# Performance work log

Hardware: AMD Instinct MI355X
Metric: run time of the kernel (lower is better)

Reference implementation:

```python
import jax, jax.numpy as jnp
import numpy as np

D_IN = 1024
D_OUT = 1024


def setup_inputs() -> dict:
    key = jax.random.key(0)
    ks = jax.random.split(key, 7)
    x = jax.random.normal(ks[0], (4, 2048, D_IN), dtype=jnp.float32)
    scale = 1.0 / np.sqrt(D_IN)
    Wq = jax.random.normal(ks[1], (D_IN, D_OUT), dtype=jnp.float32) * scale
    Wk = jax.random.normal(ks[2], (D_IN, D_OUT), dtype=jnp.float32) * scale
    Wv = jax.random.normal(ks[3], (D_IN, D_OUT), dtype=jnp.float32) * scale
    bq = jax.random.normal(ks[4], (D_OUT,), dtype=jnp.float32) * 0.01
    bk = jax.random.normal(ks[5], (D_OUT,), dtype=jnp.float32) * 0.01
    bv = jax.random.normal(ks[6], (D_OUT,), dtype=jnp.float32) * 0.01
    return {"x": x, "Wq": Wq, "bq": bq, "Wk": Wk, "bk": bk, "Wv": Wv, "bv": bv}


def reference(x, Wq, bq, Wk, bk, Wv, bv):
    # x: [B, S, d_in]
    q = jnp.einsum("bsd,de->bse", x, Wq) + bq  # [B, S, d_out]
    k = jnp.einsum("bsd,de->bse", x, Wk) + bk
    v = jnp.einsum("bsd,de->bse", x, Wv) + bv
    d_out = q.shape[-1]
    scores = jnp.einsum("bqe,bke->bqk", q, k) / jnp.sqrt(jnp.float32(d_out))
    attn = jax.nn.softmax(scores, axis=-1)  # [B, S, S]
    return jnp.einsum("bqk,bke->bqe", attn, v)
```

## Files before the change

kernel.cpp:

```cpp
#include <hip/hip_runtime.h>
#include <hip/hip_bf16.h>
#include <stdint.h>

typedef __bf16 bf16x8 __attribute__((ext_vector_type(8)));
typedef __bf16 bf16x4 __attribute__((ext_vector_type(4)));
typedef float f32x4 __attribute__((ext_vector_type(4)));

#define DEV __device__ __forceinline__

DEV void gload_lds16(const void* g, void* l) {
  __builtin_amdgcn_global_load_lds((const __attribute__((address_space(1))) void*)g,
                                   (__attribute__((address_space(3))) void*)l, 16, 0, 0);
}

#define WAITV0 asm volatile("s_waitcnt vmcnt(0)" ::: "memory")
#define MFMA16x16(a, b, c) __builtin_amdgcn_mfma_f32_16x16x32_bf16(a, b, c, 0, 0, 0)

__global__ __launch_bounds__(256) void pack_x_kernel(const float* __restrict__ x,
                                                     __bf16* __restrict__ o, long n) {
  long i = ((long)blockIdx.x * 256 + threadIdx.x) * 4;
  const long stride = (long)gridDim.x * 256 * 4;
  for (; i < n; i += stride) {
    f32x4 v = *(const f32x4*)(x + i);
    bf16x4 b;
    b[0] = (__bf16)v[0]; b[1] = (__bf16)v[1]; b[2] = (__bf16)v[2]; b[3] = (__bf16)v[3];
    *(bf16x4*)(o + i) = b;
  }
}

__global__ __launch_bounds__(256) void pack_w_kernel(const float* __restrict__ Wq,
                                                     const float* __restrict__ Wk,
                                                     const float* __restrict__ Wv,
                                                     __bf16* __restrict__ Wt) {
  const int w = blockIdx.z;
  const float* W = (w == 0) ? Wq : (w == 1) ? Wk : Wv;
  const float scale = (w == 0) ? 0.03125f : 1.0f;
  const int d0 = blockIdx.x * 64;
  const int e0 = blockIdx.y * 64;
  __shared__ __bf16 T[64][72];
  const int tid = threadIdx.x;
  const int r4 = tid >> 4;
  const int c4 = (tid & 15) * 4;
#pragma unroll
  for (int p = 0; p < 4; ++p) {
    int r = r4 + p * 16;
    f32x4 v = *(const f32x4*)(W + (long)(d0 + r) * 1024 + e0 + c4);
    T[r][c4 + 0] = (__bf16)(v[0] * scale);
    T[r][c4 + 1] = (__bf16)(v[1] * scale);
    T[r][c4 + 2] = (__bf16)(v[2] * scale);
    T[r][c4 + 3] = (__bf16)(v[3] * scale);
  }
  __syncthreads();
  const int e4 = tid >> 3;
  const int dd = (tid & 7) * 8;
#pragma unroll
  for (int p = 0; p < 2; ++p) {
    int e = e4 + p * 32;
    bf16x8 ov;
#pragma unroll
    for (int j = 0; j < 8; ++j) ov[j] = T[dd + j][e];
    *(bf16x8*)(Wt + (long)w * 1048576 + (long)(e0 + e) * 1024 + d0 + dd) = ov;
  }
}

__global__ __launch_bounds__(256) void pack_bias_kernel(const float* __restrict__ bq,
                                                        const float* __restrict__ bk,
                                                        const float* __restrict__ bv,
                                                        float* __restrict__ o) {
  int i = blockIdx.x * 256 + threadIdx.x;
  if (i < 1024) o[i] = bq[i] * 0.03125f;
  else if (i < 2048) o[i] = bk[i - 1024];
  else if (i < 3072) o[i] = bv[i - 2048];
}

template <int MODE>
__global__ __launch_bounds__(256, 2) void gemm_bk32_kernel(
    const __bf16* __restrict__ A, int lda,
    const __bf16* __restrict__ B, int ldb, long long bBatchStride, int bmShift,
    const float* __restrict__ bias,
    __bf16* __restrict__ C, int ldc,
    __bf16* __restrict__ vt,
    float* __restrict__ rowpart,
    int nTiles, int nt) {
  constexpr int ABYTES = 256 * 64;
  constexpr int BUFB = ABYTES + 128 * 64;
  __shared__ __attribute__((aligned(128))) char lds[2 * BUFB];

  const int tid = threadIdx.x;
  const int lane = tid & 63;
  const int wid = tid >> 6;
  const int wm = wid >> 1, wn = wid & 1;
  const int lo = lane & 15, hi = lane >> 4;

  const int cpx = gridDim.x >> 3;
  const int bid = blockIdx.x;
  const int swz = (bid & 7) * cpx + (bid >> 3);
  const int bm = swz / nTiles, bn = swz % nTiles;

  const __bf16* Bb = B + (long long)(bm >> bmShift) * bBatchStride;

  const __bf16* gA[4]; int lA[4];
  const __bf16* gB[2]; int lB[2];
#pragma unroll
  for (int l = 0; l < 4; ++l) {
    int s = l * 256 + tid, r = s >> 2;
    int c = (s & 3) ^ ((r >> 1) & 3);
    gA[l] = A + (long long)(bm * 256 + r) * lda + c * 8;
    lA[l] = s * 16;
  }
#pragma unroll
  for (int l = 0; l < 2; ++l) {
    int s = l * 256 + tid, r = s >> 2;
    int c = (s & 3) ^ ((r >> 1) & 3);
    gB[l] = Bb + (long long)(bn * 128 + r) * ldb + c * 8;
    lB[l] = ABYTES + s * 16;
  }

  const int pch = (hi ^ ((lo >> 1) & 3)) << 4;
  int aOff[8], bOff[4];
#pragma unroll
  for (int f = 0; f < 8; ++f) aOff[f] = (wm * 128 + f * 16 + lo) * 64 + pch;
#pragma unroll
  for (int f = 0; f < 4; ++f) bOff[f] = ABYTES + (wn * 64 + f * 16 + lo) * 64 + pch;

  f32x4 acc[8][4] = {};

#define STAGE(tt, buf)                                               \
  do {                                                               \
    const long long ko_ = (long long)(tt) * 32;                      \
    char* lb_ = lds + (buf) * BUFB;                                  \
    _Pragma("unroll") for (int l = 0; l < 4; ++l)                    \
        gload_lds16(gA[l] + ko_, lb_ + lA[l]);                       \
    _Pragma("unroll") for (int l = 0; l < 2; ++l)                    \
        gload_lds16(gB[l] + ko_, lb_ + lB[l]);                       \
  } while (0)

  STAGE(0, 0);
  WAITV0;
  __builtin_amdgcn_s_barrier();
  __builtin_amdgcn_sched_barrier(0);

  for (int t = 0; t < nt; ++t) {
    if (t + 1 < nt) STAGE(t + 1, (t + 1) & 1);
    const char* base = lds + (t & 1) * BUFB;
    bf16x8 av[8], bvv[4];
#pragma unroll
    for (int f = 0; f < 4; ++f) bvv[f] = *(const bf16x8*)(base + bOff[f]);
#pragma unroll
    for (int f = 0; f < 8; ++f) av[f] = *(const bf16x8*)(base + aOff[f]);
#pragma unroll
    for (int mi = 0; mi < 8; ++mi)
#pragma unroll
      for (int ni = 0; ni < 4; ++ni)
        acc[mi][ni] = MFMA16x16(av[mi], bvv[ni], acc[mi][ni]);
    if (t + 1 < nt) {
      WAITV0;
      __builtin_amdgcn_s_barrier();
      __builtin_amdgcn_sched_barrier(0);
    }
  }
#undef STAGE

  const long long row0 = (long long)bm * 256 + wm * 128 + hi * 4;
  const long long col0 = (long long)bn * 128 + wn * 64 + lo;

  if (MODE == 1) {
    if (bn < 16) {
#pragma unroll
      for (int ni = 0; ni < 4; ++ni) {
        const long long col = col0 + ni * 16;
        const float bvs = bias[col];
#pragma unroll
        for (int mi = 0; mi < 8; ++mi)
#pragma unroll
          for (int j = 0; j < 4; ++j)
            C[(row0 + mi * 16 + j) * ldc + col] = (__bf16)(acc[mi][ni][j] + bvs);
      }
    } else {
      const int b = bm >> 3;
      __bf16* vtb = vt + (long long)b * 2097152;
      const int tbase = (bm & 7) * 256 + wm * 128 + hi * 4;
#pragma unroll
      for (int ni = 0; ni < 4; ++ni) {
        const long long e = (long long)(bn - 16) * 128 + wn * 64 + ni * 16 + lo;
        const float bvs = bias[2048 + e];
#pragma unroll
        for (int mi = 0; mi < 8; ++mi) {
          bf16x4 o;
#pragma unroll
          for (int j = 0; j < 4; ++j) o[j] = (__bf16)(acc[mi][ni][j] + bvs);
          *(bf16x4*)(vtb + e * 2048 + tbase + mi * 16) = o;
        }
      }
    }
  } else {
    float ps[8][4];
#pragma unroll
    for (int mi = 0; mi < 8; ++mi)
#pragma unroll
      for (int j = 0; j < 4; ++j) {
        float s0 = 0.f;
#pragma unroll
        for (int ni = 0; ni < 4; ++ni) {
          float e = __expf(acc[mi][ni][j]);
          acc[mi][ni][j] = e;
          s0 += e;
        }
        ps[mi][j] = s0;
      }
#pragma unroll
    for (int ni = 0; ni < 4; ++ni) {
      const long long col = col0 + ni * 16;
#pragma unroll
      for (int mi = 0; mi < 8; ++mi)
#pragma unroll
        for (int j = 0; j < 4; ++j)
          C[(row0 + mi * 16 + j) * ldc + col] = (__bf16)acc[mi][ni][j];
    }
#pragma unroll
    for (int mi = 0; mi < 8; ++mi)
#pragma unroll
      for (int j = 0; j < 4; ++j) {
        float v = ps[mi][j];
        v += __shfl_xor(v, 1);
        v += __shfl_xor(v, 2);
        v += __shfl_xor(v, 4);
        v += __shfl_xor(v, 8);
        ps[mi][j] = v;
      }
    if (lo == 0) {
      float* rp = rowpart + (long long)(bn * 2 + wn) * 8192;
#pragma unroll
      for (int mi = 0; mi < 8; ++mi) {
        f32x4 o;
#pragma unroll
        for (int j = 0; j < 4; ++j) o[j] = ps[mi][j];
        *(f32x4*)(rp + row0 + mi * 16) = o;
      }
    }
  }
}

__global__ __launch_bounds__(256) void rowsum_kernel(const float* __restrict__ rowpart,
                                                     float* __restrict__ rowinv) {
  int r = blockIdx.x * 256 + threadIdx.x;
  float s = 0.f;
#pragma unroll
  for (int p = 0; p < 32; ++p) s += rowpart[p * 8192 + r];
  rowinv[r] = 1.0f / s;
}

__global__ __launch_bounds__(256, 2) void gemm_pv_kernel(
    const __bf16* __restrict__ A, int lda,
    const __bf16* __restrict__ B, int ldb, long long bBatchStride, int bmShift,
    const float* __restrict__ rowinv,
    float* __restrict__ C, int ldc,
    int nTiles, int nt) {
  constexpr int TILEB = 16384;
  __shared__ __attribute__((aligned(128))) char lds[2 * 2 * TILEB];

  const int tid = threadIdx.x;
  const int lane = tid & 63;
  const int wid = tid >> 6;
  const int wm = wid >> 1, wn = wid & 1;
  const int lo = lane & 15, hi = lane >> 4;

  const int cpx = gridDim.x >> 3;
  const int bid = blockIdx.x;
  const int swz = (bid & 7) * cpx + (bid >> 3);
  const int bm = swz / nTiles, bn = swz % nTiles;

  const __bf16* Bb = B + (long long)(bm >> bmShift) * bBatchStride;

  const __bf16* gA[4]; const __bf16* gB[4]; int lA[4];
#pragma unroll
  for (int l = 0; l < 4; ++l) {
    int s = l * 256 + tid, r = s >> 3;
    int c = (s & 7) ^ (r & 7);
    gA[l] = A + (long long)(bm * 128 + r) * lda + c * 8;
    gB[l] = Bb + (long long)(bn * 128 + r) * ldb + c * 8;
    lA[l] = s * 16;
  }

  const int c0 = ((0 * 4 + hi) ^ (lo & 7)) << 4;
  const int c1 = ((1 * 4 + hi) ^ (lo & 7)) << 4;
  const int aBase = (wm * 64 + lo) * 128;
  const int bBase = TILEB + (wn * 64 + lo) * 128;

  f32x4 acc[4][4] = {};

#define STAGE(tt, buf)                                                \
  do {                                                                \
    const long long ko_ = (long long)(tt) * 64;                       \
    char* lb_ = lds + (buf) * (2 * TILEB);                            \
    _Pragma("unroll") for (int l = 0; l < 4; ++l) {                   \
      gload_lds16(gA[l] + ko_, lb_ + lA[l]);                          \
      gload_lds16(gB[l] + ko_, lb_ + TILEB + lA[l]);                  \
    }                                                                 \
  } while (0)

  STAGE(0, 0);
  WAITV0;
  __builtin_amdgcn_s_barrier();
  __builtin_amdgcn_sched_barrier(0);

  for (int t = 0; t < nt; ++t) {
    if (t + 1 < nt) STAGE(t + 1, (t + 1) & 1);
    const char* base = lds + (t & 1) * (2 * TILEB);
    bf16x8 av[4][2], bv[4][2];
#pragma unroll
    for (int f = 0; f < 4; ++f) {
      av[f][0] = *(const bf16x8*)(base + aBase + f * 16 * 128 + c0);
      av[f][1] = *(const bf16x8*)(base + aBase + f * 16 * 128 + c1);
      bv[f][0] = *(const bf16x8*)(base + bBase + f * 16 * 128 + c0);
      bv[f][1] = *(const bf16x8*)(base + bBase + f * 16 * 128 + c1);
    }
#pragma unroll
    for (int mi = 0; mi < 4; ++mi)
#pragma unroll
      for (int ni = 0; ni < 4; ++ni) {
        acc[mi][ni] = MFMA16x16(av[mi][0], bv[ni][0], acc[mi][ni]);
        acc[mi][ni] = MFMA16x16(av[mi][1], bv[ni][1], acc[mi][ni]);
      }
    if (t + 1 < nt) {
      WAITV0;
      __builtin_amdgcn_s_barrier();
      __builtin_amdgcn_sched_barrier(0);
    }
  }
#undef STAGE

  const long long row0 = (long long)bm * 128 + wm * 64 + hi * 4;
  const long long col0 = (long long)bn * 128 + wn * 64 + lo;
#pragma unroll
  for (int mi = 0; mi < 4; ++mi) {
    f32x4 ri = *(const f32x4*)(rowinv + row0 + mi * 16);
#pragma unroll
    for (int ni = 0; ni < 4; ++ni) {
      const long long col = col0 + ni * 16;
#pragma unroll
      for (int j = 0; j < 4; ++j)
        C[(row0 + mi * 16 + j) * ldc + col] = acc[mi][ni][j] * ri[j];
    }
  }
}

extern "C" void kernel_launch(void* const* d_in, const int* in_sizes, int n_in,
                              void* d_out, int out_size, void* d_ws, size_t ws_size,
                              hipStream_t stream) {
  (void)in_sizes; (void)n_in; (void)out_size;
  const float* x  = (const float*)d_in[0];
  const float* Wq = (const float*)d_in[1];
  const float* bq = (const float*)d_in[2];
  const float* Wk = (const float*)d_in[3];
  const float* bk = (const float*)d_in[4];
  const float* Wv = (const float*)d_in[5];
  const float* bv = (const float*)d_in[6];
  float* out = (float*)d_out;
  char* ws = (char*)d_ws;
  if (ws_size < 124825600ULL) return;

  __bf16* x16   = (__bf16*)(ws + 0);
  __bf16* Wt    = (__bf16*)(ws + 16777216);
  float*  bqkv  = (float*)(ws + 23068672);
  __bf16* QKV   = (__bf16*)(ws + 23080960);
  __bf16* Vt    = (__bf16*)(ws + 73412608);
  __bf16* S     = (__bf16*)(ws + 90189824);
  float*  rowpt = (float*)(ws + 123744256);
  float*  rowiv = (float*)(ws + 124792832);

  pack_x_kernel<<<2048, 256, 0, stream>>>(x, x16, 8388608L);
  pack_w_kernel<<<dim3(16, 16, 3), 256, 0, stream>>>(Wq, Wk, Wv, Wt);
  pack_bias_kernel<<<12, 256, 0, stream>>>(bq, bk, bv, bqkv);

  gemm_bk32_kernel<1><<<dim3(768), 256, 0, stream>>>(
      x16, 1024, Wt, 1024, 0LL, 30, bqkv, QKV, 3072, Vt, nullptr, 24, 32);

  gemm_bk32_kernel<2><<<dim3(512), 256, 0, stream>>>(
      QKV, 3072, QKV + 1024, 3072, 6291456LL, 3, nullptr, S, 2048, nullptr, rowpt, 16, 32);

  rowsum_kernel<<<32, 256, 0, stream>>>(rowpt, rowiv);

  gemm_pv_kernel<<<dim3(512), 256, 0, stream>>>(
      S, 2048, Vt, 2048, 2097152LL, 4, rowiv, out, 1024, 8, 32);
}
```

Measured before the change: 174.0 us.

## Switch QKV and score GEMMs to 128x128 tiles with BK=64

The shared GEMM kernel changes from a 256x128 tile with K-step 32 to a 128x128 tile with K-step 64 and a new XOR swizzle over 8 chunks per row. Each warp now computes a 64x64 block with half the accumulators, and the grid sizes double, giving more blocks and fewer main-loop iterations. The aim is better occupancy and load balance across CUs at the cost of lower arithmetic intensity per block. Mode numbering is shuffled and an unused fp32-output mode is added.

```diff
diff --git a/kernel.cpp b/kernel.cpp
--- a/kernel.cpp
+++ b/kernel.cpp
@@ -74,17 +74,16 @@
 }
 
 template <int MODE>
-__global__ __launch_bounds__(256, 2) void gemm_bk32_kernel(
+__global__ __launch_bounds__(256, 2) void gemm128_kernel(
     const __bf16* __restrict__ A, int lda,
     const __bf16* __restrict__ B, int ldb, long long bBatchStride, int bmShift,
     const float* __restrict__ bias,
-    __bf16* __restrict__ C, int ldc,
+    void* __restrict__ C, int ldc,
     __bf16* __restrict__ vt,
     float* __restrict__ rowpart,
     int nTiles, int nt) {
-  constexpr int ABYTES = 256 * 64;
-  constexpr int BUFB = ABYTES + 128 * 64;
-  __shared__ __attribute__((aligned(128))) char lds[2 * BUFB];
+  constexpr int TILEB = 16384;
+  __shared__ __attribute__((aligned(128))) char lds[2 * 2 * TILEB];
 
   const int tid = threadIdx.x;
   const int lane = tid & 63;
@@ -99,40 +98,31 @@
 
   const __bf16* Bb = B + (long long)(bm >> bmShift) * bBatchStride;
 
-  const __bf16* gA[4]; int lA[4];
-  const __bf16* gB[2]; int lB[2];
+  const __bf16* gA[4]; const __bf16* gB[4]; int lA[4];
 #pragma unroll
   for (int l = 0; l < 4; ++l) {
-    int s = l * 256 + tid, r = s >> 2;
-    int c = (s & 3) ^ ((r >> 1) & 3);
-    gA[l] = A + (long long)(bm * 256 + r) * lda + c * 8;
+    int s = l * 256 + tid, r = s >> 3;
+    int c = (s & 7) ^ (r & 7);
+    gA[l] = A + (long long)(bm * 128 + r) * lda + c * 8;
+    gB[l] = Bb + (long long)(bn * 128 + r) * ldb + c * 8;
     lA[l] = s * 16;
   }
-#pragma unroll
-  for (int l = 0; l < 2; ++l) {
-    int s = l * 256 + tid, r = s >> 2;
-    int c = (s & 3) ^ ((r >> 1) & 3);
-    gB[l] = Bb + (long long)(bn * 128 + r) * ldb + c * 8;
-    lB[l] = ABYTES + s * 16;
-  }
-
-  const int pch = (hi ^ ((lo >> 1) & 3)) << 4;
-  int aOff[8], bOff[4];
-#pragma unroll
-  for (int f = 0; f < 8; ++f) aOff[f] = (wm * 128 + f * 16 + lo) * 64 + pch;
-#pragma unroll
-  for (int f = 0; f < 4; ++f) bOff[f] = ABYTES + (wn * 64 + f * 16 + lo) * 64 + pch;
-
-  f32x4 acc[8][4] = {};
-
-#define STAGE(tt, buf)                                               \
-  do {                                                               \
-    const long long ko_ = (long long)(tt) * 32;                      \
-    char* lb_ = lds + (buf) * BUFB;                                  \
-    _Pragma("unroll") for (int l = 0; l < 4; ++l)                    \
-        gload_lds16(gA[l] + ko_, lb_ + lA[l]);                       \
-    _Pragma("unroll") for (int l = 0; l < 2; ++l)                    \
-        gload_lds16(gB[l] + ko_, lb_ + lB[l]);                       \
+
+  const int c0 = ((0 * 4 + hi) ^ (lo & 7)) << 4;
+  const int c1 = ((1 * 4 + hi) ^ (lo & 7)) << 4;
+  const int aBase = (wm * 64 + lo) * 128;
+  const int bBase = TILEB + (wn * 64 + lo) * 128;
+
+  f32x4 acc[4][4] = {};
+
+#define STAGE(tt, buf)                                                \
+  do {                                                                \
+    const long long ko_ = (long long)(tt) * 64;                       \
+    char* lb_ = lds + (buf) * (2 * TILEB);                            \
+    _Pragma("unroll") for (int l = 0; l < 4; ++l) {                   \
+      gload_lds16(gA[l] + ko_, lb_ + lA[l]);                          \
+      gload_lds16(gB[l] + ko_, lb_ + TILEB + lA[l]);                  \
+    }                                                                 \
   } while (0)
 
   STAGE(0, 0);
@@ -142,17 +132,24 @@
 
   for (int t = 0; t < nt; ++t) {
     if (t + 1 < nt) STAGE(t + 1, (t + 1) & 1);
-    const char* base = lds + (t & 1) * BUFB;
-    bf16x8 av[8], bvv[4];
-#pragma unroll
-    for (int f = 0; f < 4; ++f) bvv[f] = *(const bf16x8*)(base + bOff[f]);
-#pragma unroll
-    for (int f = 0; f < 8; ++f) av[f] = *(const bf16x8*)(base + aOff[f]);
-#pragma unroll
-    for (int mi = 0; mi < 8; ++mi)
-#pragma unroll
-      for (int ni = 0; ni < 4; ++ni)
-        acc[mi][ni] = MFMA16x16(av[mi], bvv[ni], acc[mi][ni]);
+    const char* base = lds + (t & 1) * (2 * TILEB);
+
+    bf16x8 av[4][2], bv[4][2];
+#pragma unroll
+    for (int f = 0; f < 4; ++f) {
+      av[f][0] = *(const bf16x8*)(base + aBase + f * 16 * 128 + c0);
+      av[f][1] = *(const bf16x8*)(base + aBase + f * 16 * 128 + c1);
+      bv[f][0] = *(const bf16x8*)(base + bBase + f * 16 * 128 + c0);
+      bv[f][1] = *(const bf16x8*)(base + bBase + f * 16 * 128 + c1);
+    }
+#pragma unroll
+    for (int mi = 0; mi < 4; ++mi)
+#pragma unroll
+      for (int ni = 0; ni < 4; ++ni) {
+        acc[mi][ni] = MFMA16x16(av[mi][0], bv[ni][0], acc[mi][ni]);
+        acc[mi][ni] = MFMA16x16(av[mi][1], bv[ni][1], acc[mi][ni]);
+      }
+
     if (t + 1 < nt) {
       WAITV0;
       __builtin_amdgcn_s_barrier();
@@ -161,42 +158,55 @@
   }
 #undef STAGE
 
-  const long long row0 = (long long)bm * 256 + wm * 128 + hi * 4;
+  const long long row0 = (long long)bm * 128 + wm * 64 + hi * 4;
   const long long col0 = (long long)bn * 128 + wn * 64 + lo;
 
-  if (MODE == 1) {
+  if (MODE == 0) {
+    float* Cf = (float*)C;
+#pragma unroll
+    for (int ni = 0; ni < 4; ++ni) {
+      const long long col = col0 + ni * 16;
+#pragma unroll
+      for (int mi = 0; mi < 4; ++mi)
+#pragma unroll
+        for (int j = 0; j < 4; ++j)
+          Cf[(row0 + mi * 16 + j) * ldc + col] = acc[mi][ni][j];
+    }
+  } else if (MODE == 2) {
     if (bn < 16) {
+      __bf16* Ch = (__bf16*)C;
 #pragma unroll
       for (int ni = 0; ni < 4; ++ni) {
         const long long col = col0 + ni * 16;
         const float bvs = bias[col];
 #pragma unroll
-        for (int mi = 0; mi < 8; ++mi)
+        for (int mi = 0; mi < 4; ++mi)
 #pragma unroll
           for (int j = 0; j < 4; ++j)
-            C[(row0 + mi * 16 + j) * ldc + col] = (__bf16)(acc[mi][ni][j] + bvs);
+            Ch[(row0 + mi * 16 + j) * ldc + col] = (__bf16)(acc[mi][ni][j] + bvs);
       }
     } else {
-      const int b = bm >> 3;
+      const int b = bm >> 4;
       __bf16* vtb = vt + (long long)b * 2097152;
-      const int tbase = (bm & 7) * 256 + wm * 128 + hi * 4;
+      const int t0 = (bm & 15) * 128 + wm * 64 + hi * 4;
 #pragma unroll
       for (int ni = 0; ni < 4; ++ni) {
         const long long e = (long long)(bn - 16) * 128 + wn * 64 + ni * 16 + lo;
         const float bvs = bias[2048 + e];
 #pragma unroll
-        for (int mi = 0; mi < 8; ++mi) {
+        for (int mi = 0; mi < 4; ++mi) {
           bf16x4 o;
 #pragma unroll
           for (int j = 0; j < 4; ++j) o[j] = (__bf16)(acc[mi][ni][j] + bvs);
-          *(bf16x4*)(vtb + e * 2048 + tbase + mi * 16) = o;
+          *(bf16x4*)(vtb + e * 2048 + t0 + mi * 16) = o;
         }
       }
     }
   } else {
-    float ps[8][4];
-#pragma unroll
-    for (int mi = 0; mi < 8; ++mi)
+    __bf16* Ch = (__bf16*)C;
+    float ps[4][4];
+#pragma unroll
+    for (int mi = 0; mi < 4; ++mi)
 #pragma unroll
       for (int j = 0; j < 4; ++j) {
         float s0 = 0.f;
@@ -212,13 +222,13 @@
     for (int ni = 0; ni < 4; ++ni) {
       const long long col = col0 + ni * 16;
 #pragma unroll
-      for (int mi = 0; mi < 8; ++mi)
+      for (int mi = 0; mi < 4; ++mi)
 #pragma unroll
         for (int j = 0; j < 4; ++j)
-          C[(row0 + mi * 16 + j) * ldc + col] = (__bf16)acc[mi][ni][j];
-    }
-#pragma unroll
-    for (int mi = 0; mi < 8; ++mi)
+          Ch[(row0 + mi * 16 + j) * ldc + col] = (__bf16)acc[mi][ni][j];
+    }
+#pragma unroll
+    for (int mi = 0; mi < 4; ++mi)
 #pragma unroll
       for (int j = 0; j < 4; ++j) {
         float v = ps[mi][j];
@@ -231,7 +241,7 @@
     if (lo == 0) {
       float* rp = rowpart + (long long)(bn * 2 + wn) * 8192;
 #pragma unroll
-      for (int mi = 0; mi < 8; ++mi) {
+      for (int mi = 0; mi < 4; ++mi) {
         f32x4 o;
 #pragma unroll
         for (int j = 0; j < 4; ++j) o[j] = ps[mi][j];
@@ -373,11 +383,11 @@
   pack_w_kernel<<<dim3(16, 16, 3), 256, 0, stream>>>(Wq, Wk, Wv, Wt);
   pack_bias_kernel<<<12, 256, 0, stream>>>(bq, bk, bv, bqkv);
 
-  gemm_bk32_kernel<1><<<dim3(768), 256, 0, stream>>>(
-      x16, 1024, Wt, 1024, 0LL, 30, bqkv, QKV, 3072, Vt, nullptr, 24, 32);
-
-  gemm_bk32_kernel<2><<<dim3(512), 256, 0, stream>>>(
-      QKV, 3072, QKV + 1024, 3072, 6291456LL, 3, nullptr, S, 2048, nullptr, rowpt, 16, 32);
+  gemm128_kernel<2><<<dim3(1536), 256, 0, stream>>>(
+      x16, 1024, Wt, 1024, 0LL, 30, bqkv, QKV, 3072, Vt, nullptr, 24, 16);
+
+  gemm128_kernel<3><<<dim3(1024), 256, 0, stream>>>(
+      QKV, 3072, QKV + 1024, 3072, 6291456LL, 4, nullptr, S, 2048, nullptr, rowpt, 16, 16);
 
   rowsum_kernel<<<32, 256, 0, stream>>>(rowpt, rowiv);
 
```

Measured after the change: 160.7 us. 1.08x faster.
